# Kernel optimization log

Measured on AMD Instinct MI355X. Metric: run time of the kernel, lower is better.

Reference implementation:

```python
import jax, jax.numpy as jnp
import numpy as np

BETA = 0.5
ITERS = 20


def bjorck_orthonormalize(w, beta, iters):
    def body(w, _):
        wtw = jnp.matmul(w.T, w)            # [in, in]
        w = (1.0 + beta) * w - beta * jnp.matmul(w, wtw)
        return w, None
    w, _ = jax.lax.scan(body, w, None, length=iters)
    return w


def setup_inputs() -> dict:
    key = jax.random.key(0)
    k1, k2, k3 = jax.random.split(key, 3)
    x = jax.random.normal(k1, (4, 8192, 1024), dtype=jnp.float32)
    kernel = jax.random.normal(k2, (1024, 1024), dtype=jnp.float32)
    bias = jax.random.normal(k3, (1024,), dtype=jnp.float32)
    return {"x": x, "kernel": kernel, "bias": bias}


def reference(x, kernel, bias):
    # safe Bjorck scaling: sqrt(in_features * out_features)
    scaling = jnp.sqrt(jnp.asarray(kernel.shape[0] * kernel.shape[1], dtype=kernel.dtype))
    w = bjorck_orthonormalize(kernel / scaling, BETA, ITERS)  # [in, out]
    y = jnp.einsum('bsi,io->bso', x, w)
    y = y + bias.reshape((1, 1, -1))
    return y
```

## Files before the change

kernel.cpp:

```cpp
#include <hip/hip_runtime.h>
#include <cstdint>

typedef _Float16 half8 __attribute__((ext_vector_type(8)));
typedef _Float16 half4v __attribute__((ext_vector_type(4)));
typedef float f32x4 __attribute__((ext_vector_type(4)));

__device__ __forceinline__ void async_copy16(const void* g, void* l) {
    __builtin_amdgcn_global_load_lds((const __attribute__((address_space(1))) void*)g,
                                     (__attribute__((address_space(3))) void*)l, 16, 0, 0);
}

__global__ __launch_bounds__(256) void prep_w(const float* __restrict__ K,
                                              _Float16* __restrict__ w0,
                                              _Float16* __restrict__ w0T) {
    __shared__ float tile[64][65];
    const int t  = threadIdx.x;
    const int bi = blockIdx.y * 64;
    const int bj = blockIdx.x * 64;
    const int r0 = t >> 4;
    const int c4 = (t & 15) * 4;
#pragma unroll
    for (int rr = 0; rr < 4; ++rr) {
        int r = r0 + rr * 16;
        f32x4 v = *(const f32x4*)&K[(size_t)(bi + r) * 1024 + bj + c4];
        v *= 0.03125f;
        half4v h;
        h[0] = (_Float16)v[0]; h[1] = (_Float16)v[1];
        h[2] = (_Float16)v[2]; h[3] = (_Float16)v[3];
        *(half4v*)&w0[(size_t)(bi + r) * 1024 + bj + c4] = h;
        tile[r][c4 + 0] = v[0]; tile[r][c4 + 1] = v[1];
        tile[r][c4 + 2] = v[2]; tile[r][c4 + 3] = v[3];
    }
    __syncthreads();
    const int cT = t >> 4;
    const int rT = (t & 15) * 4;
#pragma unroll
    for (int cc = 0; cc < 4; ++cc) {
        int c = cT + cc * 16;
        half4v h;
        h[0] = (_Float16)tile[rT + 0][c]; h[1] = (_Float16)tile[rT + 1][c];
        h[2] = (_Float16)tile[rT + 2][c]; h[3] = (_Float16)tile[rT + 3][c];
        *(half4v*)&w0T[(size_t)(bj + c) * 1024 + bi + rT] = h;
    }
}

template <int EPI>
__global__ __launch_bounds__(256) void gemm1k(const _Float16* __restrict__ A,
                                              const _Float16* __restrict__ BT,
                                              const _Float16* __restrict__ wcur,
                                              _Float16* __restrict__ out,
                                              _Float16* __restrict__ outT) {
    __shared__ _Float16 sA[2][64 * 64];
    __shared__ _Float16 sB[2][64 * 64];
    const int t   = threadIdx.x;
    const int m0  = blockIdx.y * 64, n0 = blockIdx.x * 64;
    const int ln  = t & 63, wv = t >> 6;
    const int wm  = wv >> 1, wn = wv & 1;
    const int q   = ln >> 4, l15 = ln & 15;

    f32x4 acc[2][2];
#pragma unroll
    for (int i = 0; i < 2; ++i)
#pragma unroll
        for (int j = 0; j < 2; ++j) {
            acc[i][j][0] = 0.f; acc[i][j][1] = 0.f;
            acc[i][j][2] = 0.f; acc[i][j][3] = 0.f;
        }

    auto stage = [&](int buf, int k0) {
#pragma unroll
        for (int rnd = 0; rnd < 2; ++rnd) {
            int c = t + rnd * 256;
            int row = c >> 3, s = c & 7;
            int gs = s ^ (row & 7);
            async_copy16(A + (size_t)(m0 + row) * 1024 + k0 + gs * 8, &sA[buf][c * 8]);
            async_copy16(BT + (size_t)(n0 + row) * 1024 + k0 + gs * 8, &sB[buf][c * 8]);
        }
    };

    auto frag = [&](const _Float16* s, int row, int kc) -> half8 {
        return *(const half8*)&s[row * 64 + ((kc ^ (row & 7)) << 3)];
    };

    stage(0, 0);
    int cur = 0;
#pragma unroll 1
    for (int it = 0; it < 16; ++it) {
        __syncthreads();
        if (it < 15) stage(cur ^ 1, (it + 1) * 64);
#pragma unroll
        for (int kk = 0; kk < 2; ++kk) {
            half8 a0 = frag(sA[cur], wm * 32 + 0  + l15, kk * 4 + q);
            half8 a1 = frag(sA[cur], wm * 32 + 16 + l15, kk * 4 + q);
            half8 b0 = frag(sB[cur], wn * 32 + 0  + l15, kk * 4 + q);
            half8 b1 = frag(sB[cur], wn * 32 + 16 + l15, kk * 4 + q);
            acc[0][0] = __builtin_amdgcn_mfma_f32_16x16x32_f16(a0, b0, acc[0][0], 0, 0, 0);
            acc[0][1] = __builtin_amdgcn_mfma_f32_16x16x32_f16(a0, b1, acc[0][1], 0, 0, 0);
            acc[1][0] = __builtin_amdgcn_mfma_f32_16x16x32_f16(a1, b0, acc[1][0], 0, 0, 0);
            acc[1][1] = __builtin_amdgcn_mfma_f32_16x16x32_f16(a1, b1, acc[1][1], 0, 0, 0);
        }
        cur ^= 1;
    }

#pragma unroll
    for (int im = 0; im < 2; ++im)
#pragma unroll
        for (int jn = 0; jn < 2; ++jn) {
            int row0 = m0 + wm * 32 + im * 16 + q * 4;
            int col  = n0 + wn * 32 + jn * 16 + l15;
            if (EPI == 0) {
#pragma unroll
                for (int r = 0; r < 4; ++r)
                    out[(size_t)(row0 + r) * 1024 + col] = (_Float16)acc[im][jn][r];
            } else {
                half4v hT;
#pragma unroll
                for (int r = 0; r < 4; ++r) {
                    float w0v = (float)wcur[(size_t)(row0 + r) * 1024 + col];
                    float nv  = 1.5f * w0v - 4.8828125e-4f * acc[im][jn][r];
                    _Float16 h = (_Float16)nv;
                    out[(size_t)(row0 + r) * 1024 + col] = h;
                    hT[r] = h;
                }
                *(half4v*)&outT[(size_t)col * 1024 + row0] = hT;
            }
        }
}

__global__ __launch_bounds__(256) void gemm_big(const float* __restrict__ X,
                                                const _Float16* __restrict__ BT,
                                                const float* __restrict__ bias,
                                                float* __restrict__ Y) {
    __shared__ _Float16 sA[2][128 * 40];
    __shared__ _Float16 sB[2][128 * 32];
    const int t  = threadIdx.x;
    const int m0 = blockIdx.y * 128, n0 = blockIdx.x * 128;
    const int ln = t & 63, wv = t >> 6;
    const int wm = wv >> 1, wn = wv & 1;
    const int q  = ln >> 4, l15 = ln & 15;

    f32x4 acc[4][4];
#pragma unroll
    for (int i = 0; i < 4; ++i)
#pragma unroll
        for (int j = 0; j < 4; ++j) {
            acc[i][j][0] = 0.f; acc[i][j][1] = 0.f;
            acc[i][j][2] = 0.f; acc[i][j][3] = 0.f;
        }

    auto loadA = [&](int k0, f32x4* va) {
#pragma unroll
        for (int rnd = 0; rnd < 4; ++rnd) {
            int c = t + rnd * 256;
            int row = c >> 3, s4 = c & 7;
            va[rnd] = *(const f32x4*)&X[(size_t)(m0 + row) * 1024 + k0 + s4 * 4];
        }
    };
    auto writeA = [&](int buf, const f32x4* va) {
#pragma unroll
        for (int rnd = 0; rnd < 4; ++rnd) {
            int c = t + rnd * 256;
            int row = c >> 3, s4 = c & 7;
            half4v h;
            h[0] = (_Float16)va[rnd][0]; h[1] = (_Float16)va[rnd][1];
            h[2] = (_Float16)va[rnd][2]; h[3] = (_Float16)va[rnd][3];
            *(half4v*)&sA[buf][row * 40 + s4 * 4] = h;
        }
    };
    auto stageB = [&](int buf, int k0) {
#pragma unroll
        for (int rnd = 0; rnd < 2; ++rnd) {
            int c = t + rnd * 256;
            int row = c >> 2, s = c & 3;
            int gs = s ^ ((row >> 1) & 3);
            async_copy16(BT + (size_t)(n0 + row) * 1024 + k0 + gs * 8, &sB[buf][c * 8]);
        }
    };

    f32x4 va[4];
    loadA(0, va);
    stageB(0, 0);
    writeA(0, va);
    int cur = 0;
#pragma unroll 1
    for (int it = 0; it < 32; ++it) {
        __syncthreads();
        if (it < 31) {
            loadA((it + 1) * 32, va);
            stageB(cur ^ 1, (it + 1) * 32);
        }
        half8 a[4], b[4];
#pragma unroll
        for (int im = 0; im < 4; ++im) {
            int row = wm * 64 + im * 16 + l15;
            a[im] = *(const half8*)&sA[cur][row * 40 + q * 8];
        }
#pragma unroll
        for (int jn = 0; jn < 4; ++jn) {
            int row = wn * 64 + jn * 16 + l15;
            b[jn] = *(const half8*)&sB[cur][row * 32 + ((q ^ ((row >> 1) & 3)) << 3)];
        }
#pragma unroll
        for (int im = 0; im < 4; ++im)
#pragma unroll
            for (int jn = 0; jn < 4; ++jn)
                acc[im][jn] = __builtin_amdgcn_mfma_f32_16x16x32_f16(a[im], b[jn], acc[im][jn], 0, 0, 0);
        if (it < 31) writeA(cur ^ 1, va);
        cur ^= 1;
    }

#pragma unroll
    for (int jn = 0; jn < 4; ++jn) {
        int col = n0 + wn * 64 + jn * 16 + l15;
        float bv = bias[col];
#pragma unroll
        for (int im = 0; im < 4; ++im) {
            int row0 = m0 + wm * 64 + im * 16 + q * 4;
#pragma unroll
            for (int r = 0; r < 4; ++r)
                Y[(size_t)(row0 + r) * 1024 + col] = acc[im][jn][r] * 0.03125f + bv;
        }
    }
}

extern "C" void kernel_launch(void* const* d_in, const int* in_sizes, int n_in,
                              void* d_out, int out_size, void* d_ws, size_t ws_size,
                              hipStream_t stream) {
    (void)in_sizes; (void)n_in; (void)out_size; (void)ws_size;
    const float* x    = (const float*)d_in[0];
    const float* kern = (const float*)d_in[1];
    const float* bias = (const float*)d_in[2];
    float* y = (float*)d_out;

    char* ws = (char*)d_ws;
    const size_t SZ = (size_t)1024 * 1024 * sizeof(_Float16);
    _Float16* wh[2] = {(_Float16*)(ws + 0 * SZ), (_Float16*)(ws + 1 * SZ)};
    _Float16* wT[2] = {(_Float16*)(ws + 2 * SZ), (_Float16*)(ws + 3 * SZ)};
    _Float16* Sh    = (_Float16*)(ws + 4 * SZ);

    prep_w<<<dim3(16, 16), 256, 0, stream>>>(kern, wh[0], wT[0]);

    for (int it = 0; it < 20; ++it) {
        int c = it & 1, n = c ^ 1;
        gemm1k<0><<<dim3(16, 16), 256, 0, stream>>>(wT[c], wT[c], nullptr, Sh, nullptr);
        gemm1k<1><<<dim3(16, 16), 256, 0, stream>>>(wh[c], Sh, wh[c], wh[n], wT[n]);
    }
    gemm_big<<<dim3(8, 256), 256, 0, stream>>>(x, wT[0], bias, y);
}
```

Measured before the change: 837.1 us.

## Rework 1k GEMM with 8-wave blocks, K=128 stages, XCD-aware tile mapping

The small 1024x1024 GEMMs used by the Bjorck iterations now run 512-thread blocks. Each wave computes a 16x32 sub-tile, and the K dimension is staged in 128-wide chunks with a 16-way XOR swizzle, so there are half as many barriers per tile. The block index is remapped so that tiles sharing rows or columns land on the same XCD, which is meant to improve L2 reuse. The big GEMM grid is also transposed so consecutive blocks walk along M for a fixed N column of weights. The cost is fewer MFMAs per wave relative to LDS fragment loads and larger LDS usage per block.

```diff
diff --git a/kernel.cpp b/kernel.cpp
--- a/kernel.cpp
+++ b/kernel.cpp
@@ -45,86 +45,81 @@
 }
 
 template <int EPI>
-__global__ __launch_bounds__(256) void gemm1k(const _Float16* __restrict__ A,
+__global__ __launch_bounds__(512) void gemm1k(const _Float16* __restrict__ A,
                                               const _Float16* __restrict__ BT,
                                               const _Float16* __restrict__ wcur,
                                               _Float16* __restrict__ out,
                                               _Float16* __restrict__ outT) {
-    __shared__ _Float16 sA[2][64 * 64];
-    __shared__ _Float16 sB[2][64 * 64];
-    const int t   = threadIdx.x;
-    const int m0  = blockIdx.y * 64, n0 = blockIdx.x * 64;
-    const int ln  = t & 63, wv = t >> 6;
-    const int wm  = wv >> 1, wn = wv & 1;
-    const int q   = ln >> 4, l15 = ln & 15;
-
-    f32x4 acc[2][2];
-#pragma unroll
-    for (int i = 0; i < 2; ++i)
-#pragma unroll
-        for (int j = 0; j < 2; ++j) {
-            acc[i][j][0] = 0.f; acc[i][j][1] = 0.f;
-            acc[i][j][2] = 0.f; acc[i][j][3] = 0.f;
-        }
+    __shared__ _Float16 sA[2][8192];
+    __shared__ _Float16 sB[2][8192];
+    const int t = threadIdx.x;
+    const int b = blockIdx.x;
+    const int xcd = b & 7, j = b >> 3;
+    const int m0 = (((xcd & 1) << 3) + (j & 7)) << 6;
+    const int n0 = (((xcd >> 1) << 2) + (j >> 3)) << 6;
+    const int ln = t & 63, wv = t >> 6;
+    const int wm = wv >> 1, wn = wv & 1;
+    const int q  = ln >> 4, l15 = ln & 15;
+
+    f32x4 acc[2];
+#pragma unroll
+    for (int jn = 0; jn < 2; ++jn) {
+        acc[jn][0] = 0.f; acc[jn][1] = 0.f;
+        acc[jn][2] = 0.f; acc[jn][3] = 0.f;
+    }
 
     auto stage = [&](int buf, int k0) {
 #pragma unroll
         for (int rnd = 0; rnd < 2; ++rnd) {
-            int c = t + rnd * 256;
-            int row = c >> 3, s = c & 7;
-            int gs = s ^ (row & 7);
+            int c = t + rnd * 512;
+            int row = c >> 4, g = c & 15;
+            int gs = g ^ (row & 15);
             async_copy16(A + (size_t)(m0 + row) * 1024 + k0 + gs * 8, &sA[buf][c * 8]);
             async_copy16(BT + (size_t)(n0 + row) * 1024 + k0 + gs * 8, &sB[buf][c * 8]);
         }
     };
-
     auto frag = [&](const _Float16* s, int row, int kc) -> half8 {
-        return *(const half8*)&s[row * 64 + ((kc ^ (row & 7)) << 3)];
+        return *(const half8*)&s[row * 128 + ((kc ^ (row & 15)) << 3)];
     };
 
     stage(0, 0);
     int cur = 0;
 #pragma unroll 1
-    for (int it = 0; it < 16; ++it) {
+    for (int it = 0; it < 8; ++it) {
         __syncthreads();
-        if (it < 15) stage(cur ^ 1, (it + 1) * 64);
-#pragma unroll
-        for (int kk = 0; kk < 2; ++kk) {
-            half8 a0 = frag(sA[cur], wm * 32 + 0  + l15, kk * 4 + q);
-            half8 a1 = frag(sA[cur], wm * 32 + 16 + l15, kk * 4 + q);
+        if (it < 7) stage(cur ^ 1, (it + 1) * 128);
+#pragma unroll
+        for (int kk = 0; kk < 4; ++kk) {
+            half8 a0 = frag(sA[cur], wm * 16 + l15, kk * 4 + q);
             half8 b0 = frag(sB[cur], wn * 32 + 0  + l15, kk * 4 + q);
             half8 b1 = frag(sB[cur], wn * 32 + 16 + l15, kk * 4 + q);
-            acc[0][0] = __builtin_amdgcn_mfma_f32_16x16x32_f16(a0, b0, acc[0][0], 0, 0, 0);
-            acc[0][1] = __builtin_amdgcn_mfma_f32_16x16x32_f16(a0, b1, acc[0][1], 0, 0, 0);
-            acc[1][0] = __builtin_amdgcn_mfma_f32_16x16x32_f16(a1, b0, acc[1][0], 0, 0, 0);
-            acc[1][1] = __builtin_amdgcn_mfma_f32_16x16x32_f16(a1, b1, acc[1][1], 0, 0, 0);
+            acc[0] = __builtin_amdgcn_mfma_f32_16x16x32_f16(a0, b0, acc[0], 0, 0, 0);
+            acc[1] = __builtin_amdgcn_mfma_f32_16x16x32_f16(a0, b1, acc[1], 0, 0, 0);
         }
         cur ^= 1;
     }
 
-#pragma unroll
-    for (int im = 0; im < 2; ++im)
-#pragma unroll
-        for (int jn = 0; jn < 2; ++jn) {
-            int row0 = m0 + wm * 32 + im * 16 + q * 4;
-            int col  = n0 + wn * 32 + jn * 16 + l15;
-            if (EPI == 0) {
-#pragma unroll
-                for (int r = 0; r < 4; ++r)
-                    out[(size_t)(row0 + r) * 1024 + col] = (_Float16)acc[im][jn][r];
-            } else {
-                half4v hT;
-#pragma unroll
-                for (int r = 0; r < 4; ++r) {
-                    float w0v = (float)wcur[(size_t)(row0 + r) * 1024 + col];
-                    float nv  = 1.5f * w0v - 4.8828125e-4f * acc[im][jn][r];
-                    _Float16 h = (_Float16)nv;
-                    out[(size_t)(row0 + r) * 1024 + col] = h;
-                    hT[r] = h;
-                }
-                *(half4v*)&outT[(size_t)col * 1024 + row0] = hT;
+    const int row0 = m0 + wm * 16 + q * 4;
+#pragma unroll
+    for (int jn = 0; jn < 2; ++jn) {
+        int col = n0 + wn * 32 + jn * 16 + l15;
+        if (EPI == 0) {
+#pragma unroll
+            for (int r = 0; r < 4; ++r)
+                out[(size_t)(row0 + r) * 1024 + col] = (_Float16)acc[jn][r];
+        } else {
+            half4v hT;
+#pragma unroll
+            for (int r = 0; r < 4; ++r) {
+                float w0v = (float)wcur[(size_t)(row0 + r) * 1024 + col];
+                float nv  = 1.5f * w0v - 4.8828125e-4f * acc[jn][r];
+                _Float16 h = (_Float16)nv;
+                out[(size_t)(row0 + r) * 1024 + col] = h;
+                hT[r] = h;
             }
-        }
+            *(half4v*)&outT[(size_t)col * 1024 + row0] = hT;
+        }
+    }
 }
 
 __global__ __launch_bounds__(256) void gemm_big(const float* __restrict__ X,
@@ -134,7 +129,7 @@
     __shared__ _Float16 sA[2][128 * 40];
     __shared__ _Float16 sB[2][128 * 32];
     const int t  = threadIdx.x;
-    const int m0 = blockIdx.y * 128, n0 = blockIdx.x * 128;
+    const int m0 = blockIdx.x * 128, n0 = blockIdx.y * 128;
     const int ln = t & 63, wv = t >> 6;
     const int wm = wv >> 1, wn = wv & 1;
     const int q  = ln >> 4, l15 = ln & 15;
@@ -242,8 +237,8 @@
 
     for (int it = 0; it < 20; ++it) {
         int c = it & 1, n = c ^ 1;
-        gemm1k<0><<<dim3(16, 16), 256, 0, stream>>>(wT[c], wT[c], nullptr, Sh, nullptr);
-        gemm1k<1><<<dim3(16, 16), 256, 0, stream>>>(wh[c], Sh, wh[c], wh[n], wT[n]);
-    }
-    gemm_big<<<dim3(8, 256), 256, 0, stream>>>(x, wT[0], bias, y);
-}
+        gemm1k<0><<<256, 512, 0, stream>>>(wT[c], wT[c], nullptr, Sh, nullptr);
+        gemm1k<1><<<256, 512, 0, stream>>>(wh[c], Sh, wh[c], wh[n], wT[n]);
+    }
+    gemm_big<<<dim3(256, 8), 256, 0, stream>>>(x, wT[0], bias, y);
+}
```

New measurement: 743.0 us. 1.13x faster.
